# Optimization experiments

Hardware: AMD Instinct MI355X
Metric: run time of the kernel (lower is better)

## Reference

```python
import jax, jax.numpy as jnp
import numpy as np

M = 4                 # margin order (init kwarg m=4)
LAMB = 1000.0         # it=0: max(lambda_min, lambda_max/(1+gamma*0)**power) = 1000
B, D, C = 512, 256, 100000


def setup_inputs() -> dict:
    key = jax.random.key(0)
    k1, k2, k3 = jax.random.split(key, 3)
    x = jax.random.normal(k1, (B, D), dtype=jnp.float32)
    # kaiming_uniform_(weight, a=1.0): bound = sqrt(6/((1+a^2)*fan_in)) = sqrt(3/D)
    bound = float(np.sqrt(3.0 / D))
    weight = jax.random.uniform(k2, (C, D), dtype=jnp.float32, minval=-bound, maxval=bound)
    y = jax.random.randint(k3, (B,), 0, C)
    return {"x": x, "weight": weight, "y": y}


def reference(x, weight, y):
    # weight row-normalization (normalize=True path, done in-place in torch)
    wl = jnp.sqrt(jnp.sum(weight * weight, axis=1, keepdims=True))
    w = weight / wl                                  # (C, D), unit rows -> wlen == 1
    xlen = jnp.sqrt(jnp.sum(x * x, axis=1, keepdims=True))   # (B, 1)
    cos = jnp.clip((x @ w.T) / xlen, -1.0, 1.0)      # (B, C) cos_theta
    # m=4 Chebyshev: cos(4t) = 8c^4 - 8c^2 + 1
    c2 = cos * cos
    cos_m = 8.0 * c2 * c2 - 8.0 * c2 + 1.0
    k = jnp.floor(M * jnp.arccos(cos) / jnp.pi)      # (B, C)
    sign = 1.0 - 2.0 * (k % 2.0)                     # (-1)**k
    phi = sign * cos_m - 2.0 * k
    feat = cos * xlen
    onehot = jax.nn.one_hot(y, w.shape[0], dtype=feat.dtype)  # (B, C)
    # at label positions: feat <- (lamb*feat + phi*xlen) / (1+lamb)
    feat = feat + onehot * ((phi * xlen - feat) / (1.0 + LAMB))
    return feat
```

## Files before the change

kernel.cpp:

```cpp
#include <hip/hip_runtime.h>
#include <hip/hip_bf16.h>

#define B_DIM 512
#define D_DIM 256
#define C_DIM 100000
#define LAMB 1000.0f

using bf16x8 = __attribute__((ext_vector_type(8))) short;
using f32x4  = __attribute__((ext_vector_type(4))) float;

__device__ __forceinline__ short f2bf(float f) {
  unsigned u = __builtin_bit_cast(unsigned, f);
  u += 0x7FFFu + ((u >> 16) & 1u);
  return (short)(u >> 16);
}

__device__ __forceinline__ void gload_lds16(const void* g, void* l) {
  __builtin_amdgcn_global_load_lds(
      (__attribute__((address_space(1))) void*)g,
      (__attribute__((address_space(3))) void*)l, 16, 0, 0);
}

__global__ __launch_bounds__(256) void prep_x(const float* __restrict__ x,
                                              unsigned short* __restrict__ x_swz,
                                              float* __restrict__ xlen) {
  int wv = threadIdx.x >> 6, lane = threadIdx.x & 63;
  int row = blockIdx.x * 4 + wv;
  float4 v = *(const float4*)(x + row * D_DIM + lane * 4);
  float ss = v.x * v.x + v.y * v.y + v.z * v.z + v.w * v.w;
#pragma unroll
  for (int m = 1; m < 64; m <<= 1) ss += __shfl_xor(ss, m);
  if (lane == 0) xlen[row] = sqrtf(ss);
  ushort4 u;
  u.x = (unsigned short)f2bf(v.x);
  u.y = (unsigned short)f2bf(v.y);
  u.z = (unsigned short)f2bf(v.z);
  u.w = (unsigned short)f2bf(v.w);
  int byteoff = row * 512 + ((lane * 8) ^ ((row & 7) << 4));
  *(ushort4*)((char*)x_swz + byteoff) = u;
}

__global__ __launch_bounds__(256) void gemm_bf16(
    const float* __restrict__ W, const unsigned short* __restrict__ xb,
    const float* __restrict__ xlen, float* __restrict__ out) {
  __shared__ unsigned short xs[2][32 * 256];
  __shared__ float xlen_s[B_DIM];

  const int tid = threadIdx.x;
  const int lane = tid & 63, wv = tid >> 6;
  const int l15 = lane & 15, g = lane >> 4;
  const int bn0 = blockIdx.x * 128 + wv * 32;

  for (int i = tid; i < B_DIM; i += 256) xlen_s[i] = xlen[i];

#pragma unroll
  for (int i = 0; i < 4; ++i)
    gload_lds16((const char*)xb + i * 4096 + tid * 16,
                (char*)xs[0] + i * 4096 + wv * 1024);

  bf16x8 fw[2][8];
  float invw4[2][4];
#pragma unroll
  for (int it = 0; it < 2; ++it) {
    int col = bn0 + it * 16 + l15;
    if (col >= C_DIM) col = C_DIM - 1;
    const float* wr = W + (size_t)col * D_DIM + g * 8;
    float ss = 0.f;
#pragma unroll
    for (int kg = 0; kg < 8; ++kg) {
      float4 a = *(const float4*)(wr + kg * 32);
      float4 b = *(const float4*)(wr + kg * 32 + 4);
      ss += a.x * a.x + a.y * a.y + a.z * a.z + a.w * a.w
          + b.x * b.x + b.y * b.y + b.z * b.z + b.w * b.w;
      bf16x8 f;
      f[0] = f2bf(a.x); f[1] = f2bf(a.y); f[2] = f2bf(a.z); f[3] = f2bf(a.w);
      f[4] = f2bf(b.x); f[5] = f2bf(b.y); f[6] = f2bf(b.z); f[7] = f2bf(b.w);
      fw[it][kg] = f;
    }
    ss += __shfl_xor(ss, 16);
    ss += __shfl_xor(ss, 32);
    float iw = 1.0f / sqrtf(ss);
#pragma unroll
    for (int r = 0; r < 4; ++r) invw4[it][r] = __shfl(iw, g * 4 + r);
  }

  __syncthreads();

  int buf = 0;
  for (int chunk = 0; chunk < 16; ++chunk) {
    if (chunk < 15) {
#pragma unroll
      for (int i = 0; i < 4; ++i)
        gload_lds16((const char*)xb + (chunk + 1) * 16384 + i * 4096 + tid * 16,
                    (char*)xs[buf ^ 1] + i * 4096 + wv * 1024);
    }

#pragma unroll
    for (int jtl = 0; jtl < 2; ++jtl) {
      const int xrow = chunk * 32 + jtl * 16 + l15;
      const float xl = xlen_s[xrow];
      const char* xp = (const char*)xs[buf] + (jtl * 16 + l15) * 512;
      const int swz = (l15 & 7) << 4;
      bf16x8 fx[8];
#pragma unroll
      for (int kg = 0; kg < 8; ++kg)
        fx[kg] = *(const bf16x8*)(xp + ((kg * 64 + g * 16) ^ swz));

      f32x4 acc0 = {}, acc1 = {};
#pragma unroll
      for (int kg = 0; kg < 8; ++kg) {
        acc0 = __builtin_amdgcn_mfma_f32_16x16x32_bf16(fw[0][kg], fx[kg], acc0, 0, 0, 0);
        acc1 = __builtin_amdgcn_mfma_f32_16x16x32_bf16(fw[1][kg], fx[kg], acc1, 0, 0, 0);
      }

#pragma unroll
      for (int it = 0; it < 2; ++it) {
        const f32x4& a = it ? acc1 : acc0;
        int wc = bn0 + it * 16 + g * 4;
        if (wc < C_DIM) {
          float4 v;
          v.x = fminf(fmaxf(a[0] * invw4[it][0], -xl), xl);
          v.y = fminf(fmaxf(a[1] * invw4[it][1], -xl), xl);
          v.z = fminf(fmaxf(a[2] * invw4[it][2], -xl), xl);
          v.w = fminf(fmaxf(a[3] * invw4[it][3], -xl), xl);
          *(float4*)(out + (size_t)xrow * C_DIM + wc) = v;
        }
      }
    }

    __syncthreads();
    buf ^= 1;
  }
}

__global__ __launch_bounds__(256) void fix_labels(const float* __restrict__ x,
                                                  const float* __restrict__ W,
                                                  const int* __restrict__ y,
                                                  float* __restrict__ out) {
  int wv = threadIdx.x >> 6, lane = threadIdx.x & 63;
  int b = blockIdx.x * 4 + wv;
  int c = y[b];
  float4 wvv = *(const float4*)(W + (size_t)c * D_DIM + lane * 4);
  float4 xv  = *(const float4*)(x + b * D_DIM + lane * 4);
  float dt = wvv.x * xv.x + wvv.y * xv.y + wvv.z * xv.z + wvv.w * xv.w;
  float sw = wvv.x * wvv.x + wvv.y * wvv.y + wvv.z * wvv.z + wvv.w * wvv.w;
  float sx = xv.x * xv.x + xv.y * xv.y + xv.z * xv.z + xv.w * xv.w;
#pragma unroll
  for (int m = 1; m < 64; m <<= 1) {
    dt += __shfl_xor(dt, m);
    sw += __shfl_xor(sw, m);
    sx += __shfl_xor(sx, m);
  }
  if (lane == 0) {
    float xl = sqrtf(sx), wl = sqrtf(sw);
    float cth = dt / (xl * wl);
    cth = fminf(fmaxf(cth, -1.f), 1.f);
    float c2 = cth * cth;
    float cm = 8.f * c2 * c2 - 8.f * c2 + 1.f;
    float k = floorf(4.0f * acosf(cth) / 3.14159265358979323846f);
    float sgn = (((int)k) & 1) ? -1.f : 1.f;
    float phi = sgn * cm - 2.f * k;
    float feat = cth * xl;
    out[(size_t)b * C_DIM + c] = feat + (phi * xl - feat) / (1.f + LAMB);
  }
}

extern "C" void kernel_launch(void* const* d_in, const int* in_sizes, int n_in,
                              void* d_out, int out_size, void* d_ws, size_t ws_size,
                              hipStream_t stream) {
  const float* x = (const float*)d_in[0];
  const float* W = (const float*)d_in[1];
  const int*   y = (const int*)d_in[2];
  float* out = (float*)d_out;

  unsigned short* xb = (unsigned short*)d_ws;
  float* xlen = (float*)((char*)d_ws + B_DIM * D_DIM * 2);

  prep_x<<<B_DIM / 4, 256, 0, stream>>>(x, xb, xlen);
  gemm_bf16<<<(C_DIM + 127) / 128, 256, 0, stream>>>(W, xb, xlen, out);
  fix_labels<<<B_DIM / 4, 256, 0, stream>>>(x, W, y, out);
}
```

Baseline: 95.53 us.

## Use persistent GEMM blocks with atomic tile queue over split row halves

Replaces the one-block-per-128-column-panel launch with 1024 persistent blocks that pull tiles from a global atomic counter. Each tile covers a 128-column panel and half of the 512 batch rows, which doubles the tile count for better load balance across CUs. The counter is reset inside prep_x. The cost is that W panels are loaded and converted twice, plus extra atomics and syncs per tile, in exchange for less tail imbalance and steadier output write streaming.

```diff
diff --git a/kernel.cpp b/kernel.cpp
--- a/kernel.cpp
+++ b/kernel.cpp
@@ -5,6 +5,8 @@
 #define D_DIM 256
 #define C_DIM 100000
 #define LAMB 1000.0f
+#define NPANEL 782
+#define NTILE (NPANEL * 2)
 
 using bf16x8 = __attribute__((ext_vector_type(8))) short;
 using f32x4  = __attribute__((ext_vector_type(4))) float;
@@ -23,7 +25,9 @@
 
 __global__ __launch_bounds__(256) void prep_x(const float* __restrict__ x,
                                               unsigned short* __restrict__ x_swz,
-                                              float* __restrict__ xlen) {
+                                              float* __restrict__ xlen,
+                                              unsigned int* __restrict__ ctr) {
+  if (blockIdx.x == 0 && threadIdx.x == 0) *ctr = 0u;
   int wv = threadIdx.x >> 6, lane = threadIdx.x & 63;
   int row = blockIdx.x * 4 + wv;
   float4 v = *(const float4*)(x + row * D_DIM + lane * 4);
@@ -42,94 +46,108 @@
 
 __global__ __launch_bounds__(256) void gemm_bf16(
     const float* __restrict__ W, const unsigned short* __restrict__ xb,
-    const float* __restrict__ xlen, float* __restrict__ out) {
+    const float* __restrict__ xlen, unsigned int* __restrict__ ctr,
+    float* __restrict__ out) {
   __shared__ unsigned short xs[2][32 * 256];
   __shared__ float xlen_s[B_DIM];
+  __shared__ unsigned int t_s;
 
   const int tid = threadIdx.x;
   const int lane = tid & 63, wv = tid >> 6;
   const int l15 = lane & 15, g = lane >> 4;
-  const int bn0 = blockIdx.x * 128 + wv * 32;
 
   for (int i = tid; i < B_DIM; i += 256) xlen_s[i] = xlen[i];
 
-#pragma unroll
-  for (int i = 0; i < 4; ++i)
-    gload_lds16((const char*)xb + i * 4096 + tid * 16,
-                (char*)xs[0] + i * 4096 + wv * 1024);
-
-  bf16x8 fw[2][8];
-  float invw4[2][4];
-#pragma unroll
-  for (int it = 0; it < 2; ++it) {
-    int col = bn0 + it * 16 + l15;
-    if (col >= C_DIM) col = C_DIM - 1;
-    const float* wr = W + (size_t)col * D_DIM + g * 8;
-    float ss = 0.f;
-#pragma unroll
-    for (int kg = 0; kg < 8; ++kg) {
-      float4 a = *(const float4*)(wr + kg * 32);
-      float4 b = *(const float4*)(wr + kg * 32 + 4);
-      ss += a.x * a.x + a.y * a.y + a.z * a.z + a.w * a.w
-          + b.x * b.x + b.y * b.y + b.z * b.z + b.w * b.w;
-      bf16x8 f;
-      f[0] = f2bf(a.x); f[1] = f2bf(a.y); f[2] = f2bf(a.z); f[3] = f2bf(a.w);
-      f[4] = f2bf(b.x); f[5] = f2bf(b.y); f[6] = f2bf(b.z); f[7] = f2bf(b.w);
-      fw[it][kg] = f;
+  for (;;) {
+    if (tid == 0) t_s = atomicAdd(ctr, 1u);
+    __syncthreads();
+    const unsigned t = t_s;
+    if (t >= NTILE) break;
+    const int panel = t >> 1, half = t & 1;
+    const int bn0 = panel * 128 + wv * 32;
+    const int row0 = half * 256;
+
+#pragma unroll
+    for (int i = 0; i < 4; ++i)
+      gload_lds16((const char*)xb + row0 * 512 + i * 4096 + tid * 16,
+                  (char*)xs[0] + i * 4096 + wv * 1024);
+
+    bf16x8 fw[2][8];
+    float invw4[2][4];
+#pragma unroll
+    for (int it = 0; it < 2; ++it) {
+      int col = bn0 + it * 16 + l15;
+      if (col >= C_DIM) col = C_DIM - 1;
+      const float* wr = W + (size_t)col * D_DIM + g * 8;
+      float ss = 0.f;
+#pragma unroll
+      for (int kg = 0; kg < 8; ++kg) {
+        float4 a = *(const float4*)(wr + kg * 32);
+        float4 b = *(const float4*)(wr + kg * 32 + 4);
+        ss += a.x * a.x + a.y * a.y + a.z * a.z + a.w * a.w
+            + b.x * b.x + b.y * b.y + b.z * b.z + b.w * b.w;
+        bf16x8 f;
+        f[0] = f2bf(a.x); f[1] = f2bf(a.y); f[2] = f2bf(a.z); f[3] = f2bf(a.w);
+        f[4] = f2bf(b.x); f[5] = f2bf(b.y); f[6] = f2bf(b.z); f[7] = f2bf(b.w);
+        fw[it][kg] = f;
+      }
+      ss += __shfl_xor(ss, 16);
+      ss += __shfl_xor(ss, 32);
+      float iw = 1.0f / sqrtf(ss);
+#pragma unroll
+      for (int r = 0; r < 4; ++r) invw4[it][r] = __shfl(iw, g * 4 + r);
     }
-    ss += __shfl_xor(ss, 16);
-    ss += __shfl_xor(ss, 32);
-    float iw = 1.0f / sqrtf(ss);
-#pragma unroll
-    for (int r = 0; r < 4; ++r) invw4[it][r] = __shfl(iw, g * 4 + r);
-  }
-
-  __syncthreads();
-
-  int buf = 0;
-  for (int chunk = 0; chunk < 16; ++chunk) {
-    if (chunk < 15) {
-#pragma unroll
-      for (int i = 0; i < 4; ++i)
-        gload_lds16((const char*)xb + (chunk + 1) * 16384 + i * 4096 + tid * 16,
-                    (char*)xs[buf ^ 1] + i * 4096 + wv * 1024);
-    }
-
-#pragma unroll
-    for (int jtl = 0; jtl < 2; ++jtl) {
-      const int xrow = chunk * 32 + jtl * 16 + l15;
-      const float xl = xlen_s[xrow];
-      const char* xp = (const char*)xs[buf] + (jtl * 16 + l15) * 512;
-      const int swz = (l15 & 7) << 4;
-      bf16x8 fx[8];
-#pragma unroll
-      for (int kg = 0; kg < 8; ++kg)
-        fx[kg] = *(const bf16x8*)(xp + ((kg * 64 + g * 16) ^ swz));
-
-      f32x4 acc0 = {}, acc1 = {};
-#pragma unroll
-      for (int kg = 0; kg < 8; ++kg) {
-        acc0 = __builtin_amdgcn_mfma_f32_16x16x32_bf16(fw[0][kg], fx[kg], acc0, 0, 0, 0);
-        acc1 = __builtin_amdgcn_mfma_f32_16x16x32_bf16(fw[1][kg], fx[kg], acc1, 0, 0, 0);
+
+    __syncthreads();
+
+    int buf = 0;
+    for (int chunk = 0; chunk < 8; ++chunk) {
+      if (chunk < 7) {
+#pragma unroll
+        for (int i = 0; i < 4; ++i)
+          gload_lds16((const char*)xb + row0 * 512 + (chunk + 1) * 16384 +
+                          i * 4096 + tid * 16,
+                      (char*)xs[buf ^ 1] + i * 4096 + wv * 1024);
       }
 
 #pragma unroll
-      for (int it = 0; it < 2; ++it) {
-        const f32x4& a = it ? acc1 : acc0;
-        int wc = bn0 + it * 16 + g * 4;
-        if (wc < C_DIM) {
-          float4 v;
-          v.x = fminf(fmaxf(a[0] * invw4[it][0], -xl), xl);
-          v.y = fminf(fmaxf(a[1] * invw4[it][1], -xl), xl);
-          v.z = fminf(fmaxf(a[2] * invw4[it][2], -xl), xl);
-          v.w = fminf(fmaxf(a[3] * invw4[it][3], -xl), xl);
-          *(float4*)(out + (size_t)xrow * C_DIM + wc) = v;
+      for (int jtl = 0; jtl < 2; ++jtl) {
+        const int lr = jtl * 16 + l15;
+        const int row = row0 + chunk * 32 + lr;
+        const float xl = xlen_s[row];
+        const char* xp = (const char*)xs[buf] + lr * 512;
+        const int swz = (l15 & 7) << 4;
+        bf16x8 fx[8];
+#pragma unroll
+        for (int kg = 0; kg < 8; ++kg)
+          fx[kg] = *(const bf16x8*)(xp + ((kg * 64 + g * 16) ^ swz));
+
+        f32x4 acc0 = {}, acc1 = {};
+#pragma unroll
+        for (int kg = 0; kg < 8; ++kg) {
+          acc0 = __builtin_amdgcn_mfma_f32_16x16x32_bf16(fw[0][kg], fx[kg], acc0, 0, 0, 0);
+          acc1 = __builtin_amdgcn_mfma_f32_16x16x32_bf16(fw[1][kg], fx[kg], acc1, 0, 0, 0);
+        }
+
+        const size_t orow = (size_t)row * C_DIM;
+#pragma unroll
+        for (int it = 0; it < 2; ++it) {
+          const f32x4& a = it ? acc1 : acc0;
+          int wc = bn0 + it * 16 + g * 4;
+          if (wc < C_DIM) {
+            float4 v;
+            v.x = fminf(fmaxf(a[0] * invw4[it][0], -xl), xl);
+            v.y = fminf(fmaxf(a[1] * invw4[it][1], -xl), xl);
+            v.z = fminf(fmaxf(a[2] * invw4[it][2], -xl), xl);
+            v.w = fminf(fmaxf(a[3] * invw4[it][3], -xl), xl);
+            *(float4*)(out + orow + wc) = v;
+          }
         }
       }
+
+      __syncthreads();
+      buf ^= 1;
     }
-
-    __syncthreads();
-    buf ^= 1;
   }
 }
 
@@ -175,8 +193,9 @@
 
   unsigned short* xb = (unsigned short*)d_ws;
   float* xlen = (float*)((char*)d_ws + B_DIM * D_DIM * 2);
-
-  prep_x<<<B_DIM / 4, 256, 0, stream>>>(x, xb, xlen);
-  gemm_bf16<<<(C_DIM + 127) / 128, 256, 0, stream>>>(W, xb, xlen, out);
+  unsigned int* ctr = (unsigned int*)((char*)d_ws + B_DIM * D_DIM * 2 + 2048);
+
+  prep_x<<<B_DIM / 4, 256, 0, stream>>>(x, xb, xlen, ctr);
+  gemm_bf16<<<1024, 256, 0, stream>>>(W, xb, xlen, ctr, out);
   fix_labels<<<B_DIM / 4, 256, 0, stream>>>(x, W, y, out);
 }
```

After: 101.4 us. 1.06x slower.

## Split GEMM into 256-column panels by two row halves with rotated chunk order

Applied to the files above, without the earlier changes.

Each block now has 512 threads covering 256 weight columns, and only half of the 512 batch rows. Two blocks share a column panel, one per row half. The starting x chunk is rotated by block id so concurrently running blocks write to different output rows at the same time, which is meant to spread write traffic across memory channels. The cost is that each weight column is loaded and normalized twice (once per half), and there are fewer blocks per column.

```diff
diff --git a/kernel.cpp b/kernel.cpp
--- a/kernel.cpp
+++ b/kernel.cpp
@@ -5,6 +5,7 @@
 #define D_DIM 256
 #define C_DIM 100000
 #define LAMB 1000.0f
+#define NPANEL 391
 
 using bf16x8 = __attribute__((ext_vector_type(8))) short;
 using f32x4  = __attribute__((ext_vector_type(4))) float;
@@ -40,23 +41,29 @@
   *(ushort4*)((char*)x_swz + byteoff) = u;
 }
 
-__global__ __launch_bounds__(256) void gemm_bf16(
+__global__ __launch_bounds__(512) void gemm_bf16(
     const float* __restrict__ W, const unsigned short* __restrict__ xb,
     const float* __restrict__ xlen, float* __restrict__ out) {
   __shared__ unsigned short xs[2][32 * 256];
-  __shared__ float xlen_s[B_DIM];
+  __shared__ float xlen_s[256];
 
   const int tid = threadIdx.x;
   const int lane = tid & 63, wv = tid >> 6;
   const int l15 = lane & 15, g = lane >> 4;
-  const int bn0 = blockIdx.x * 128 + wv * 32;
 
-  for (int i = tid; i < B_DIM; i += 256) xlen_s[i] = xlen[i];
+  const int bid = blockIdx.x;
+  const int panel = bid >> 1, half = bid & 1;
+  const int bn0 = panel * 256 + wv * 32;
+  const int row0 = half * 256;
+
+  if (tid < 256) xlen_s[tid] = xlen[row0 + tid];
+
+#define ROT(c) (((c) + bid) & 7)
 
 #pragma unroll
-  for (int i = 0; i < 4; ++i)
-    gload_lds16((const char*)xb + i * 4096 + tid * 16,
-                (char*)xs[0] + i * 4096 + wv * 1024);
+  for (int i = 0; i < 2; ++i)
+    gload_lds16((const char*)xb + (row0 + ROT(0) * 32) * 512 + i * 8192 + tid * 16,
+                (char*)xs[0] + i * 8192 + wv * 1024);
 
   bf16x8 fw[2][8];
   float invw4[2][4];
@@ -87,19 +94,20 @@
   __syncthreads();
 
   int buf = 0;
-  for (int chunk = 0; chunk < 16; ++chunk) {
-    if (chunk < 15) {
+  for (int c = 0; c < 8; ++c) {
+    if (c < 7) {
 #pragma unroll
-      for (int i = 0; i < 4; ++i)
-        gload_lds16((const char*)xb + (chunk + 1) * 16384 + i * 4096 + tid * 16,
-                    (char*)xs[buf ^ 1] + i * 4096 + wv * 1024);
+      for (int i = 0; i < 2; ++i)
+        gload_lds16((const char*)xb + (row0 + ROT(c + 1) * 32) * 512 + i * 8192 + tid * 16,
+                    (char*)xs[buf ^ 1] + i * 8192 + wv * 1024);
     }
 
 #pragma unroll
     for (int jtl = 0; jtl < 2; ++jtl) {
-      const int xrow = chunk * 32 + jtl * 16 + l15;
-      const float xl = xlen_s[xrow];
-      const char* xp = (const char*)xs[buf] + (jtl * 16 + l15) * 512;
+      const int lr = jtl * 16 + l15;
+      const int row = row0 + ROT(c) * 32 + lr;
+      const float xl = xlen_s[row - row0];
+      const char* xp = (const char*)xs[buf] + lr * 512;
       const int swz = (l15 & 7) << 4;
       bf16x8 fx[8];
 #pragma unroll
@@ -113,6 +121,7 @@
         acc1 = __builtin_amdgcn_mfma_f32_16x16x32_bf16(fw[1][kg], fx[kg], acc1, 0, 0, 0);
       }
 
+      const size_t orow = (size_t)row * C_DIM;
 #pragma unroll
       for (int it = 0; it < 2; ++it) {
         const f32x4& a = it ? acc1 : acc0;
@@ -123,7 +132,7 @@
           v.y = fminf(fmaxf(a[1] * invw4[it][1], -xl), xl);
           v.z = fminf(fmaxf(a[2] * invw4[it][2], -xl), xl);
           v.w = fminf(fmaxf(a[3] * invw4[it][3], -xl), xl);
-          *(float4*)(out + (size_t)xrow * C_DIM + wc) = v;
+          *(float4*)(out + orow + wc) = v;
         }
       }
     }
@@ -131,6 +140,7 @@
     __syncthreads();
     buf ^= 1;
   }
+#undef ROT
 }
 
 __global__ __launch_bounds__(256) void fix_labels(const float* __restrict__ x,
@@ -177,6 +187,6 @@
   float* xlen = (float*)((char*)d_ws + B_DIM * D_DIM * 2);
 
   prep_x<<<B_DIM / 4, 256, 0, stream>>>(x, xb, xlen);
-  gemm_bf16<<<(C_DIM + 127) / 128, 256, 0, stream>>>(W, xb, xlen, out);
+  gemm_bf16<<<NPANEL * 2, 512, 0, stream>>>(W, xb, xlen, out);
   fix_labels<<<B_DIM / 4, 256, 0, stream>>>(x, W, y, out);
 }
```

Measured after the change: 109.7 us. +14.9%, slower.
